# Performance work log

Measured on AMD Instinct MI355X. Metric: run time of the kernel, lower is better.

The kernel has to match this reference:

```python
import jax, jax.numpy as jnp
import numpy as np

NEG_SLOPE = 0.2
CONV3_NUM, CONV1_NUM, POLY_NUM = 3, 5, 4
FEAT_DIM = CONV3_NUM * 84 + CONV1_NUM * 12 + POLY_NUM * 12  # 360
DN = ('NCHW', 'OIHW', 'NCHW')


def leaky_relu(x):
    return jnp.where(x >= 0, x, NEG_SLOPE * x)


def conv3x3(x, feat):
    # per-sample dynamic 3x3 conv: feat[:, :81] -> kernel [3,3,3,3], feat[:, 81:84] -> bias
    B = x.shape[0]
    k = feat[:, :81].reshape(B, 3, 3, 3, 3)
    b = feat[:, 81:84]

    def one(xi, ki, bi):
        y = jax.lax.conv_general_dilated(xi[None], ki, (1, 1), 'SAME', dimension_numbers=DN)[0]
        return y + bi[:, None, None]

    return leaky_relu(jax.vmap(one)(x, k, b))


def conv1x1(x, feat):
    B = x.shape[0]
    k = feat[:, :9].reshape(B, 3, 3, 1, 1)
    b = feat[:, 9:12]

    def one(xi, ki, bi):
        y = jax.lax.conv_general_dilated(xi[None], ki, (1, 1), 'VALID', dimension_numbers=DN)[0]
        return y + bi[:, None, None]

    return leaky_relu(jax.vmap(one)(x, k, b))


def conv_stack(x, feature):
    residual = x
    for i in range(CONV3_NUM):
        x = conv3x3(x, feature[:, i * 84:(i + 1) * 84])
    off = CONV3_NUM * 84
    for i in range(CONV1_NUM):
        x = conv1x1(x, feature[:, off + i * 12:off + (i + 1) * 12])
    return residual + x


def att_map(feat, h_mat, w_mat, xc):
    # product over POLY_NUM of (a*h + b*w + c*x + d)
    att = jnp.ones_like(xc)
    for i in range(POLY_NUM):
        a = feat[:, i * 4 + 0].reshape(-1, 1, 1, 1)
        b = feat[:, i * 4 + 1].reshape(-1, 1, 1, 1)
        c = feat[:, i * 4 + 2].reshape(-1, 1, 1, 1)
        d = feat[:, i * 4 + 3].reshape(-1, 1, 1, 1)
        att = att * (a * h_mat + b * w_mat + c * xc + d)
    return att


def apply_attention(x, feature):
    H, W = x.shape[2], x.shape[3]
    h_mat = (jnp.arange(H, dtype=x.dtype) / H).reshape(1, 1, H, 1)
    w_mat = (jnp.arange(W, dtype=x.dtype) / W).reshape(1, 1, 1, W)
    off = CONV3_NUM * 84 + CONV1_NUM * 12
    atts = [att_map(feature[:, off + c * POLY_NUM * 4: off + (c + 1) * POLY_NUM * 4],
                    h_mat, w_mat, x[:, c:c + 1]) for c in range(3)]  # R, G, B
    att = jnp.concatenate(atts, axis=1)
    return x * (1 + att)


def setup_inputs() -> dict:
    key = jax.random.key(0)
    k1, k2, k3 = jax.random.split(key, 3)
    x = jax.random.uniform(k1, (8, 3, 512, 512), dtype=jnp.float32)
    thumb_x = jax.random.uniform(k2, (8, 3, 64, 64), dtype=jnp.float32)
    Wm = jax.random.normal(k3, (3, FEAT_DIM), dtype=jnp.float32) * 0.05
    bm = jnp.zeros((FEAT_DIM,), dtype=jnp.float32)
    return {"x": x, "thumb_x": thumb_x, "Wm": Wm, "bm": bm}


def reference(x, thumb_x, Wm, bm):
    # meta: GAP over thumbnail -> linear -> per-sample hypernetwork features [B, 360]
    feature = jnp.mean(thumb_x, axis=(2, 3)) @ Wm + bm
    x = conv_stack(x, feature)
    x = apply_attention(x, feature)
    thumb = conv_stack(thumb_x, feature)
    thumb = apply_attention(thumb, feature)
    return (x, thumb)
```

## Files before the change

kernel.cpp:

```cpp
#include <hip/hip_runtime.h>


#define LEAKY(v) fmaxf((v), 0.2f * (v))

constexpr int STRD = 84;
constexpr int ROWS0 = 22;
constexpr int CHS  = ROWS0 * STRD;
constexpr int BUFSZ = 3 * CHS + 16;

__global__ __launch_bounds__(384) void prep_kernel(
    const float* __restrict__ thumb, const float* __restrict__ Wm,
    const float* __restrict__ bm, float* __restrict__ feat)
{
    const int b = blockIdx.x;
    const int t = threadIdx.x;
    const int ch = t >> 7;
    const int l  = t & 127;
    const float4* p = (const float4*)(thumb + (size_t)b * 3 * 4096);
    float s = 0.f;
#pragma unroll
    for (int k = 0; k < 8; ++k) {
        float4 v = p[ch * 1024 + l + k * 128];
        s += v.x + v.y + v.z + v.w;
    }
    __shared__ float red[384];
    red[t] = s;
    __syncthreads();
    for (int off = 64; off > 0; off >>= 1) {
        if (l < off) red[t] += red[t + off];
        __syncthreads();
    }
    if (t < 360) {
        const float sc = 1.f / 4096.f;
        const float m0 = red[0] * sc, m1 = red[128] * sc, m2 = red[256] * sc;
        feat[b * 360 + t] =
            fmaf(m0, Wm[t], fmaf(m1, Wm[360 + t], fmaf(m2, Wm[720 + t], bm[t])));
    }
}

template<int R>
__device__ __forceinline__ void conv_rows(
    const float* __restrict__ buf, const float* __restrict__ fw,
    int r0, int gx, float4 acc[][3])
{
    const float b0 = fw[81], b1 = fw[82], b2 = fw[83];
#pragma unroll
    for (int j = 0; j < R; ++j) {
        acc[j][0] = make_float4(b0, b0, b0, b0);
        acc[j][1] = make_float4(b1, b1, b1, b1);
        acc[j][2] = make_float4(b2, b2, b2, b2);
    }
    const int gA = (gx < 0) ? 0 : gx;
#pragma unroll
    for (int ich = 0; ich < 3; ++ich) {
#pragma unroll
        for (int ri = 0; ri < R + 2; ++ri) {
            const int idx = ich * CHS + (r0 + 2 + ri) * STRD;
            const float4 A = *(const float4*)&buf[idx + gA];
            const float4 B = *(const float4*)&buf[idx + gx + 4];
            const float4 C = *(const float4*)&buf[idx + gx + 8];
#pragma unroll
            for (int j = 0; j < R; ++j) {
                const int dy = ri - j;
                if (dy < 0 || dy > 2) continue;
#pragma unroll
                for (int oc = 0; oc < 3; ++oc) {
                    const float w0 = fw[oc * 27 + ich * 9 + dy * 3 + 0];
                    const float w1 = fw[oc * 27 + ich * 9 + dy * 3 + 1];
                    const float w2 = fw[oc * 27 + ich * 9 + dy * 3 + 2];
                    float4& a = acc[j][oc];
                    a.x = fmaf(A.w, w0, fmaf(B.x, w1, fmaf(B.y, w2, a.x)));
                    a.y = fmaf(B.x, w0, fmaf(B.y, w1, fmaf(B.z, w2, a.y)));
                    a.z = fmaf(B.y, w0, fmaf(B.z, w1, fmaf(B.w, w2, a.z)));
                    a.w = fmaf(B.z, w0, fmaf(B.w, w1, fmaf(C.x, w2, a.w)));
                }
            }
        }
    }
}

__global__ __launch_bounds__(256, 4) void conv_att_kernel(
    const float* __restrict__ x, const float* __restrict__ thumb,
    const float* __restrict__ feat, float* __restrict__ out)
{
    __shared__ float buf[BUFSZ];

    int id = blockIdx.x;
    const float* src; float* dst; int H, W, b, trow, tcol;
    if (id < 2048) {
        b = id >> 8; const int t = id & 255;
        H = 512; W = 512; trow = (t >> 3) * 16; tcol = (t & 7) * 64;
        src = x; dst = out;
    } else {
        const int i2 = id - 2048;
        b = i2 >> 2; trow = (i2 & 3) * 16; tcol = 0;
        H = 64; W = 64; src = thumb;
        dst = out + (size_t)8 * 3 * 512 * 512;
    }
    const float* fb = feat + b * 360;
    const int tid = threadIdx.x;

    const float* sbg = src + (size_t)b * 3 * H * W;
    for (int q = tid; q < 1188; q += 256) {
        const int c = q / 396;
        const int rem = q - c * 396;
        const int mr = rem / 18;
        const int mq = rem - mr * 18;
        const int gr = trow + mr - 3;
        const int gc0 = tcol + 4 * mq - 4;
        const bool rok = (unsigned)gr < (unsigned)H;
        const float* gp = sbg + (size_t)c * H * W + (size_t)(rok ? gr : 0) * W;
        float4 v;
        if (rok && (unsigned)gc0 <= (unsigned)(W - 4)) {
            v = *(const float4*)&gp[gc0];
        } else {
            v.x = (rok && (unsigned)(gc0 + 0) < (unsigned)W) ? gp[gc0 + 0] : 0.f;
            v.y = (rok && (unsigned)(gc0 + 1) < (unsigned)W) ? gp[gc0 + 1] : 0.f;
            v.z = (rok && (unsigned)(gc0 + 2) < (unsigned)W) ? gp[gc0 + 2] : 0.f;
            v.w = (rok && (unsigned)(gc0 + 3) < (unsigned)W) ? gp[gc0 + 3] : 0.f;
        }
        *(float4*)&buf[c * CHS + mr * STRD + 4 * mq] = v;
    }
    if (tid < 66) {
        const int c = tid / 22, mr = tid - c * 22;
        *(float4*)&buf[c * CHS + mr * STRD + 72] = make_float4(0.f, 0.f, 0.f, 0.f);
    }
    __syncthreads();

    const int s3 = tid >> 4;
    const int gx3 = 4 * (tid & 15);

    const bool act1 = tid < 180;
    const int s1 = tid / 18;
    const int gx1 = 4 * (tid - s1 * 18) - 4;
    float4 acc[2][3];
    if (act1) conv_rows<2>(buf, fb, 2 * s1 - 2, gx1, acc);

    float4 res[3];
#pragma unroll
    for (int c = 0; c < 3; ++c)
        res[c] = *(const float4*)&buf[c * CHS + (s3 + 3) * STRD + gx3 + 4];
    __syncthreads();

    if (act1) {
        const int r0 = 2 * s1 - 2;
#pragma unroll
        for (int j = 0; j < 2; ++j)
#pragma unroll
            for (int oc = 0; oc < 3; ++oc) {
                float4 v = acc[j][oc];
                v.x = LEAKY(v.x); v.y = LEAKY(v.y); v.z = LEAKY(v.z); v.w = LEAKY(v.w);
                *(float4*)&buf[oc * CHS + (r0 + j + 3) * STRD + gx1 + 4] = v;
            }
    }
    __syncthreads();

    const bool act2 = tid < 162;
    const int s2 = tid / 18;
    const int gx2 = 4 * (tid - s2 * 18) - 4;
    if (act2) conv_rows<2>(buf, fb + 84, 2 * s2 - 1, gx2, acc);
    __syncthreads();

    if (act2) {
        const int r0 = 2 * s2 - 1;
#pragma unroll
        for (int j = 0; j < 2; ++j)
#pragma unroll
            for (int oc = 0; oc < 3; ++oc) {
                float4 v = acc[j][oc];
                v.x = LEAKY(v.x); v.y = LEAKY(v.y); v.z = LEAKY(v.z); v.w = LEAKY(v.w);
                *(float4*)&buf[oc * CHS + (r0 + j + 3) * STRD + gx2 + 4] = v;
            }
    }
    __syncthreads();

    float4 y[1][3];
    conv_rows<1>(buf, fb + 168, s3, gx3, y);
    float4 y0 = y[0][0], y1 = y[0][1], y2 = y[0][2];
    y0.x = LEAKY(y0.x); y0.y = LEAKY(y0.y); y0.z = LEAKY(y0.z); y0.w = LEAKY(y0.w);
    y1.x = LEAKY(y1.x); y1.y = LEAKY(y1.y); y1.z = LEAKY(y1.z); y1.w = LEAKY(y1.w);
    y2.x = LEAKY(y2.x); y2.y = LEAKY(y2.y); y2.z = LEAKY(y2.z); y2.w = LEAKY(y2.w);

#pragma unroll
    for (int lay = 0; lay < 5; ++lay) {
        const float* fw = fb + 252 + lay * 12;
        const float w00 = fw[0], w01 = fw[1], w02 = fw[2];
        const float w10 = fw[3], w11 = fw[4], w12 = fw[5];
        const float w20 = fw[6], w21 = fw[7], w22 = fw[8];
        const float c0 = fw[9], c1 = fw[10], c2 = fw[11];
        float4 z0, z1, z2;
        z0.x = fmaf(y0.x, w00, fmaf(y1.x, w01, fmaf(y2.x, w02, c0)));
        z0.y = fmaf(y0.y, w00, fmaf(y1.y, w01, fmaf(y2.y, w02, c0)));
        z0.z = fmaf(y0.z, w00, fmaf(y1.z, w01, fmaf(y2.z, w02, c0)));
        z0.w = fmaf(y0.w, w00, fmaf(y1.w, w01, fmaf(y2.w, w02, c0)));
        z1.x = fmaf(y0.x, w10, fmaf(y1.x, w11, fmaf(y2.x, w12, c1)));
        z1.y = fmaf(y0.y, w10, fmaf(y1.y, w11, fmaf(y2.y, w12, c1)));
        z1.z = fmaf(y0.z, w10, fmaf(y1.z, w11, fmaf(y2.z, w12, c1)));
        z1.w = fmaf(y0.w, w10, fmaf(y1.w, w11, fmaf(y2.w, w12, c1)));
        z2.x = fmaf(y0.x, w20, fmaf(y1.x, w21, fmaf(y2.x, w22, c2)));
        z2.y = fmaf(y0.y, w20, fmaf(y1.y, w21, fmaf(y2.y, w22, c2)));
        z2.z = fmaf(y0.z, w20, fmaf(y1.z, w21, fmaf(y2.z, w22, c2)));
        z2.w = fmaf(y0.w, w20, fmaf(y1.w, w21, fmaf(y2.w, w22, c2)));
        y0.x = LEAKY(z0.x); y0.y = LEAKY(z0.y); y0.z = LEAKY(z0.z); y0.w = LEAKY(z0.w);
        y1.x = LEAKY(z1.x); y1.y = LEAKY(z1.y); y1.z = LEAKY(z1.z); y1.w = LEAKY(z1.w);
        y2.x = LEAKY(z2.x); y2.y = LEAKY(z2.y); y2.z = LEAKY(z2.z); y2.w = LEAKY(z2.w);
    }

    const float invH = 1.f / (float)H;
    const float invW = 1.f / (float)W;
    const int gr = trow + s3;
    const float h = (float)gr * invH;
    const float wbase = (float)(tcol + gx3) * invW;
    const float4 wv = make_float4(wbase, wbase + invW, wbase + 2.f * invW, wbase + 3.f * invW);
#pragma unroll
    for (int ch = 0; ch < 3; ++ch) {
        const float* fp = fb + 312 + ch * 16;
        const float pa0 = fp[0], pb0 = fp[1], pc0 = fp[2], pd0 = fp[3];
        const float pa1 = fp[4], pb1 = fp[5], pc1 = fp[6], pd1 = fp[7];
        const float pa2 = fp[8], pb2 = fp[9], pc2 = fp[10], pd2 = fp[11];
        const float pa3 = fp[12], pb3 = fp[13], pc3 = fp[14], pd3 = fp[15];
        const float4 yv = (ch == 0) ? y0 : (ch == 1) ? y1 : y2;
        float4 v;
        v.x = yv.x + res[ch].x;
        v.y = yv.y + res[ch].y;
        v.z = yv.z + res[ch].z;
        v.w = yv.w + res[ch].w;
        const float t0 = fmaf(pa0, h, pd0), t1 = fmaf(pa1, h, pd1);
        const float t2 = fmaf(pa2, h, pd2), t3 = fmaf(pa3, h, pd3);
        float4 o;
        float a0 = fmaf(pb0, wv.x, fmaf(pc0, v.x, t0));
        a0 *= fmaf(pb1, wv.x, fmaf(pc1, v.x, t1));
        a0 *= fmaf(pb2, wv.x, fmaf(pc2, v.x, t2));
        a0 *= fmaf(pb3, wv.x, fmaf(pc3, v.x, t3));
        o.x = v.x * (1.f + a0);
        float a1 = fmaf(pb0, wv.y, fmaf(pc0, v.y, t0));
        a1 *= fmaf(pb1, wv.y, fmaf(pc1, v.y, t1));
        a1 *= fmaf(pb2, wv.y, fmaf(pc2, v.y, t2));
        a1 *= fmaf(pb3, wv.y, fmaf(pc3, v.y, t3));
        o.y = v.y * (1.f + a1);
        float a2 = fmaf(pb0, wv.z, fmaf(pc0, v.z, t0));
        a2 *= fmaf(pb1, wv.z, fmaf(pc1, v.z, t1));
        a2 *= fmaf(pb2, wv.z, fmaf(pc2, v.z, t2));
        a2 *= fmaf(pb3, wv.z, fmaf(pc3, v.z, t3));
        o.z = v.z * (1.f + a2);
        float a3 = fmaf(pb0, wv.w, fmaf(pc0, v.w, t0));
        a3 *= fmaf(pb1, wv.w, fmaf(pc1, v.w, t1));
        a3 *= fmaf(pb2, wv.w, fmaf(pc2, v.w, t2));
        a3 *= fmaf(pb3, wv.w, fmaf(pc3, v.w, t3));
        o.w = v.w * (1.f + a3);
        *(float4*)&dst[((size_t)(b * 3 + ch) * H + gr) * W + tcol + gx3] = o;
    }
}

extern "C" void kernel_launch(void* const* d_in, const int* in_sizes, int n_in,
                              void* d_out, int out_size, void* d_ws, size_t ws_size,
                              hipStream_t stream) {
    const float* x = (const float*)d_in[0];
    const float* thumb = (const float*)d_in[1];
    const float* Wm = (const float*)d_in[2];
    const float* bm = (const float*)d_in[3];
    float* out = (float*)d_out;
    float* feat = (float*)d_ws;

    prep_kernel<<<8, 384, 0, stream>>>(thumb, Wm, bm, feat);
    conv_att_kernel<<<2080, 256, 0, stream>>>(x, thumb, feat, out);
}
```

Baseline: 114.4 us.

## Widen conv tiles to 120 columns to cut halo recompute overhead

Widens each block's tile from 64 to 120 output columns (5 column tiles per 16-row band), with a 132-float shared-memory row stride. The smaller grid gives each thread extra work passes for the first two conv layers and two passes for the final stage. The wider tile lowers the fraction of halo loads and halo recomputation across the three chained 3x3 convs. The residual is now re-read from global memory instead of being kept from shared memory, and the larger shared buffer plus partial passes may cut occupancy or add idle lanes.

```diff
diff --git a/kernel.cpp b/kernel.cpp
--- a/kernel.cpp
+++ b/kernel.cpp
@@ -3,10 +3,10 @@
 
 #define LEAKY(v) fmaxf((v), 0.2f * (v))
 
-constexpr int STRD = 84;
+constexpr int STRD = 132;
 constexpr int ROWS0 = 22;
 constexpr int CHS  = ROWS0 * STRD;
-constexpr int BUFSZ = 3 * CHS + 16;
+constexpr int BUFSZ = 3 * CHS + 4;
 
 __global__ __launch_bounds__(384) void prep_kernel(
     const float* __restrict__ thumb, const float* __restrict__ Wm,
@@ -50,15 +50,15 @@
         acc[j][1] = make_float4(b1, b1, b1, b1);
         acc[j][2] = make_float4(b2, b2, b2, b2);
     }
-    const int gA = (gx < 0) ? 0 : gx;
+    const int gA = (gx == 0) ? 0 : gx - 4;
 #pragma unroll
     for (int ich = 0; ich < 3; ++ich) {
 #pragma unroll
         for (int ri = 0; ri < R + 2; ++ri) {
             const int idx = ich * CHS + (r0 + 2 + ri) * STRD;
             const float4 A = *(const float4*)&buf[idx + gA];
-            const float4 B = *(const float4*)&buf[idx + gx + 4];
-            const float4 C = *(const float4*)&buf[idx + gx + 8];
+            const float4 B = *(const float4*)&buf[idx + gx];
+            const float4 C = *(const float4*)&buf[idx + gx + 4];
 #pragma unroll
             for (int j = 0; j < R; ++j) {
                 const int dy = ri - j;
@@ -79,6 +79,19 @@
     }
 }
 
+__device__ __forceinline__ void write_strip(
+    float* __restrict__ buf, int r0, int gx, float4 acc[][3])
+{
+#pragma unroll
+    for (int j = 0; j < 2; ++j)
+#pragma unroll
+        for (int oc = 0; oc < 3; ++oc) {
+            float4 v = acc[j][oc];
+            v.x = LEAKY(v.x); v.y = LEAKY(v.y); v.z = LEAKY(v.z); v.w = LEAKY(v.w);
+            *(float4*)&buf[oc * CHS + (r0 + j + 3) * STRD + gx] = v;
+        }
+}
+
 __global__ __launch_bounds__(256, 4) void conv_att_kernel(
     const float* __restrict__ x, const float* __restrict__ thumb,
     const float* __restrict__ feat, float* __restrict__ out)
@@ -87,12 +100,13 @@
 
     int id = blockIdx.x;
     const float* src; float* dst; int H, W, b, trow, tcol;
-    if (id < 2048) {
-        b = id >> 8; const int t = id & 255;
-        H = 512; W = 512; trow = (t >> 3) * 16; tcol = (t & 7) * 64;
+    if (id < 1280) {
+        b = id / 160; const int t = id - b * 160;
+        const int band = t / 5, ct = t - band * 5;
+        H = 512; W = 512; trow = band * 16; tcol = ct * 120;
         src = x; dst = out;
     } else {
-        const int i2 = id - 2048;
+        const int i2 = id - 1280;
         b = i2 >> 2; trow = (i2 & 3) * 16; tcol = 0;
         H = 64; W = 64; src = thumb;
         dst = out + (size_t)8 * 3 * 512 * 512;
@@ -101,11 +115,11 @@
     const int tid = threadIdx.x;
 
     const float* sbg = src + (size_t)b * 3 * H * W;
-    for (int q = tid; q < 1188; q += 256) {
-        const int c = q / 396;
-        const int rem = q - c * 396;
-        const int mr = rem / 18;
-        const int mq = rem - mr * 18;
+    for (int q = tid; q < 2178; q += 256) {
+        const int c = q / 726;
+        const int rem = q - c * 726;
+        const int mr = rem / 33;
+        const int mq = rem - mr * 33;
         const int gr = trow + mr - 3;
         const int gc0 = tcol + 4 * mq - 4;
         const bool rok = (unsigned)gr < (unsigned)H;
@@ -121,134 +135,140 @@
         }
         *(float4*)&buf[c * CHS + mr * STRD + 4 * mq] = v;
     }
-    if (tid < 66) {
-        const int c = tid / 22, mr = tid - c * 22;
-        *(float4*)&buf[c * CHS + mr * STRD + 72] = make_float4(0.f, 0.f, 0.f, 0.f);
-    }
-    __syncthreads();
-
-    const int s3 = tid >> 4;
-    const int gx3 = 4 * (tid & 15);
-
-    const bool act1 = tid < 180;
-    const int s1 = tid / 18;
-    const int gx1 = 4 * (tid - s1 * 18) - 4;
-    float4 acc[2][3];
-    if (act1) conv_rows<2>(buf, fb, 2 * s1 - 2, gx1, acc);
-
-    float4 res[3];
-#pragma unroll
-    for (int c = 0; c < 3; ++c)
-        res[c] = *(const float4*)&buf[c * CHS + (s3 + 3) * STRD + gx3 + 4];
-    __syncthreads();
-
-    if (act1) {
-        const int r0 = 2 * s1 - 2;
-#pragma unroll
-        for (int j = 0; j < 2; ++j)
-#pragma unroll
-            for (int oc = 0; oc < 3; ++oc) {
-                float4 v = acc[j][oc];
-                v.x = LEAKY(v.x); v.y = LEAKY(v.y); v.z = LEAKY(v.z); v.w = LEAKY(v.w);
-                *(float4*)&buf[oc * CHS + (r0 + j + 3) * STRD + gx1 + 4] = v;
-            }
-    }
-    __syncthreads();
-
-    const bool act2 = tid < 162;
-    const int s2 = tid / 18;
-    const int gx2 = 4 * (tid - s2 * 18) - 4;
-    if (act2) conv_rows<2>(buf, fb + 84, 2 * s2 - 1, gx2, acc);
-    __syncthreads();
-
-    if (act2) {
-        const int r0 = 2 * s2 - 1;
-#pragma unroll
-        for (int j = 0; j < 2; ++j)
-#pragma unroll
-            for (int oc = 0; oc < 3; ++oc) {
-                float4 v = acc[j][oc];
-                v.x = LEAKY(v.x); v.y = LEAKY(v.y); v.z = LEAKY(v.z); v.w = LEAKY(v.w);
-                *(float4*)&buf[oc * CHS + (r0 + j + 3) * STRD + gx2 + 4] = v;
-            }
-    }
-    __syncthreads();
-
-    float4 y[1][3];
-    conv_rows<1>(buf, fb + 168, s3, gx3, y);
-    float4 y0 = y[0][0], y1 = y[0][1], y2 = y[0][2];
-    y0.x = LEAKY(y0.x); y0.y = LEAKY(y0.y); y0.z = LEAKY(y0.z); y0.w = LEAKY(y0.w);
-    y1.x = LEAKY(y1.x); y1.y = LEAKY(y1.y); y1.z = LEAKY(y1.z); y1.w = LEAKY(y1.w);
-    y2.x = LEAKY(y2.x); y2.y = LEAKY(y2.y); y2.z = LEAKY(y2.z); y2.w = LEAKY(y2.w);
-
-#pragma unroll
-    for (int lay = 0; lay < 5; ++lay) {
-        const float* fw = fb + 252 + lay * 12;
-        const float w00 = fw[0], w01 = fw[1], w02 = fw[2];
-        const float w10 = fw[3], w11 = fw[4], w12 = fw[5];
-        const float w20 = fw[6], w21 = fw[7], w22 = fw[8];
-        const float c0 = fw[9], c1 = fw[10], c2 = fw[11];
-        float4 z0, z1, z2;
-        z0.x = fmaf(y0.x, w00, fmaf(y1.x, w01, fmaf(y2.x, w02, c0)));
-        z0.y = fmaf(y0.y, w00, fmaf(y1.y, w01, fmaf(y2.y, w02, c0)));
-        z0.z = fmaf(y0.z, w00, fmaf(y1.z, w01, fmaf(y2.z, w02, c0)));
-        z0.w = fmaf(y0.w, w00, fmaf(y1.w, w01, fmaf(y2.w, w02, c0)));
-        z1.x = fmaf(y0.x, w10, fmaf(y1.x, w11, fmaf(y2.x, w12, c1)));
-        z1.y = fmaf(y0.y, w10, fmaf(y1.y, w11, fmaf(y2.y, w12, c1)));
-        z1.z = fmaf(y0.z, w10, fmaf(y1.z, w11, fmaf(y2.z, w12, c1)));
-        z1.w = fmaf(y0.w, w10, fmaf(y1.w, w11, fmaf(y2.w, w12, c1)));
-        z2.x = fmaf(y0.x, w20, fmaf(y1.x, w21, fmaf(y2.x, w22, c2)));
-        z2.y = fmaf(y0.y, w20, fmaf(y1.y, w21, fmaf(y2.y, w22, c2)));
-        z2.z = fmaf(y0.z, w20, fmaf(y1.z, w21, fmaf(y2.z, w22, c2)));
-        z2.w = fmaf(y0.w, w20, fmaf(y1.w, w21, fmaf(y2.w, w22, c2)));
-        y0.x = LEAKY(z0.x); y0.y = LEAKY(z0.y); y0.z = LEAKY(z0.z); y0.w = LEAKY(z0.w);
-        y1.x = LEAKY(z1.x); y1.y = LEAKY(z1.y); y1.z = LEAKY(z1.z); y1.w = LEAKY(z1.w);
-        y2.x = LEAKY(z2.x); y2.y = LEAKY(z2.y); y2.z = LEAKY(z2.z); y2.w = LEAKY(z2.w);
-    }
+    __syncthreads();
+
+    float4 acc1[2][3], acc2[2][3];
+    {
+        const int s = tid >> 5, g = tid & 31;
+        conv_rows<2>(buf, fb, 2 * s - 2, 4 * g, acc1);
+    }
+    const bool p2a = tid < 64;
+    if (p2a) {
+        const int u = tid + 256;
+        const int s = u >> 5, g = u & 31;
+        conv_rows<2>(buf, fb, 2 * s - 2, 4 * g, acc2);
+    }
+    __syncthreads();
+    {
+        const int s = tid >> 5, g = tid & 31;
+        write_strip(buf, 2 * s - 2, 4 * g, acc1);
+        if (p2a) {
+            const int u = tid + 256;
+            const int s2 = u >> 5, g2 = u & 31;
+            write_strip(buf, 2 * s2 - 2, 4 * g2, acc2);
+        }
+    }
+    __syncthreads();
+
+    {
+        const int s = tid >> 5, g = tid & 31;
+        conv_rows<2>(buf, fb + 84, 2 * s - 1, 4 * g, acc1);
+    }
+    const bool p2b = tid < 32;
+    if (p2b) {
+        const int u = tid + 256;
+        const int s = u >> 5, g = u & 31;
+        conv_rows<2>(buf, fb + 84, 2 * s - 1, 4 * g, acc2);
+    }
+    __syncthreads();
+    {
+        const int s = tid >> 5, g = tid & 31;
+        write_strip(buf, 2 * s - 1, 4 * g, acc1);
+        if (p2b) {
+            const int u = tid + 256;
+            const int s2 = u >> 5, g2 = u & 31;
+            write_strip(buf, 2 * s2 - 1, 4 * g2, acc2);
+        }
+    }
+    __syncthreads();
 
     const float invH = 1.f / (float)H;
     const float invW = 1.f / (float)W;
-    const int gr = trow + s3;
-    const float h = (float)gr * invH;
-    const float wbase = (float)(tcol + gx3) * invW;
-    const float4 wv = make_float4(wbase, wbase + invW, wbase + 2.f * invW, wbase + 3.f * invW);
-#pragma unroll
-    for (int ch = 0; ch < 3; ++ch) {
-        const float* fp = fb + 312 + ch * 16;
-        const float pa0 = fp[0], pb0 = fp[1], pc0 = fp[2], pd0 = fp[3];
-        const float pa1 = fp[4], pb1 = fp[5], pc1 = fp[6], pd1 = fp[7];
-        const float pa2 = fp[8], pb2 = fp[9], pc2 = fp[10], pd2 = fp[11];
-        const float pa3 = fp[12], pb3 = fp[13], pc3 = fp[14], pd3 = fp[15];
-        const float4 yv = (ch == 0) ? y0 : (ch == 1) ? y1 : y2;
-        float4 v;
-        v.x = yv.x + res[ch].x;
-        v.y = yv.y + res[ch].y;
-        v.z = yv.z + res[ch].z;
-        v.w = yv.w + res[ch].w;
-        const float t0 = fmaf(pa0, h, pd0), t1 = fmaf(pa1, h, pd1);
-        const float t2 = fmaf(pa2, h, pd2), t3 = fmaf(pa3, h, pd3);
-        float4 o;
-        float a0 = fmaf(pb0, wv.x, fmaf(pc0, v.x, t0));
-        a0 *= fmaf(pb1, wv.x, fmaf(pc1, v.x, t1));
-        a0 *= fmaf(pb2, wv.x, fmaf(pc2, v.x, t2));
-        a0 *= fmaf(pb3, wv.x, fmaf(pc3, v.x, t3));
-        o.x = v.x * (1.f + a0);
-        float a1 = fmaf(pb0, wv.y, fmaf(pc0, v.y, t0));
-        a1 *= fmaf(pb1, wv.y, fmaf(pc1, v.y, t1));
-        a1 *= fmaf(pb2, wv.y, fmaf(pc2, v.y, t2));
-        a1 *= fmaf(pb3, wv.y, fmaf(pc3, v.y, t3));
-        o.y = v.y * (1.f + a1);
-        float a2 = fmaf(pb0, wv.z, fmaf(pc0, v.z, t0));
-        a2 *= fmaf(pb1, wv.z, fmaf(pc1, v.z, t1));
-        a2 *= fmaf(pb2, wv.z, fmaf(pc2, v.z, t2));
-        a2 *= fmaf(pb3, wv.z, fmaf(pc3, v.z, t3));
-        o.z = v.z * (1.f + a2);
-        float a3 = fmaf(pb0, wv.w, fmaf(pc0, v.w, t0));
-        a3 *= fmaf(pb1, wv.w, fmaf(pc1, v.w, t1));
-        a3 *= fmaf(pb2, wv.w, fmaf(pc2, v.w, t2));
-        a3 *= fmaf(pb3, wv.w, fmaf(pc3, v.w, t3));
-        o.w = v.w * (1.f + a3);
-        *(float4*)&dst[((size_t)(b * 3 + ch) * H + gr) * W + tcol + gx3] = o;
+#pragma unroll
+    for (int pass = 0; pass < 2; ++pass) {
+        const int u = tid + pass * 256;
+        const int s3 = u >> 5;
+        const int gq = u & 31;
+        float4 y[1][3];
+        conv_rows<1>(buf, fb + 168, s3, 4 * gq, y);
+        float4 y0 = y[0][0], y1 = y[0][1], y2 = y[0][2];
+        y0.x = LEAKY(y0.x); y0.y = LEAKY(y0.y); y0.z = LEAKY(y0.z); y0.w = LEAKY(y0.w);
+        y1.x = LEAKY(y1.x); y1.y = LEAKY(y1.y); y1.z = LEAKY(y1.z); y1.w = LEAKY(y1.w);
+        y2.x = LEAKY(y2.x); y2.y = LEAKY(y2.y); y2.z = LEAKY(y2.z); y2.w = LEAKY(y2.w);
+
+#pragma unroll
+        for (int lay = 0; lay < 5; ++lay) {
+            const float* fw = fb + 252 + lay * 12;
+            const float w00 = fw[0], w01 = fw[1], w02 = fw[2];
+            const float w10 = fw[3], w11 = fw[4], w12 = fw[5];
+            const float w20 = fw[6], w21 = fw[7], w22 = fw[8];
+            const float c0 = fw[9], c1 = fw[10], c2 = fw[11];
+            float4 z0, z1, z2;
+            z0.x = fmaf(y0.x, w00, fmaf(y1.x, w01, fmaf(y2.x, w02, c0)));
+            z0.y = fmaf(y0.y, w00, fmaf(y1.y, w01, fmaf(y2.y, w02, c0)));
+            z0.z = fmaf(y0.z, w00, fmaf(y1.z, w01, fmaf(y2.z, w02, c0)));
+            z0.w = fmaf(y0.w, w00, fmaf(y1.w, w01, fmaf(y2.w, w02, c0)));
+            z1.x = fmaf(y0.x, w10, fmaf(y1.x, w11, fmaf(y2.x, w12, c1)));
+            z1.y = fmaf(y0.y, w10, fmaf(y1.y, w11, fmaf(y2.y, w12, c1)));
+            z1.z = fmaf(y0.z, w10, fmaf(y1.z, w11, fmaf(y2.z, w12, c1)));
+            z1.w = fmaf(y0.w, w10, fmaf(y1.w, w11, fmaf(y2.w, w12, c1)));
+            z2.x = fmaf(y0.x, w20, fmaf(y1.x, w21, fmaf(y2.x, w22, c2)));
+            z2.y = fmaf(y0.y, w20, fmaf(y1.y, w21, fmaf(y2.y, w22, c2)));
+            z2.z = fmaf(y0.z, w20, fmaf(y1.z, w21, fmaf(y2.z, w22, c2)));
+            z2.w = fmaf(y0.w, w20, fmaf(y1.w, w21, fmaf(y2.w, w22, c2)));
+            y0.x = LEAKY(z0.x); y0.y = LEAKY(z0.y); y0.z = LEAKY(z0.z); y0.w = LEAKY(z0.w);
+            y1.x = LEAKY(z1.x); y1.y = LEAKY(z1.y); y1.z = LEAKY(z1.z); y1.w = LEAKY(z1.w);
+            y2.x = LEAKY(z2.x); y2.y = LEAKY(z2.y); y2.z = LEAKY(z2.z); y2.w = LEAKY(z2.w);
+        }
+
+        const int gr = trow + s3;
+        const int c0i = tcol + 4 * gq - 4;
+        if (gq >= 1 && c0i <= W - 4) {
+            const float h = (float)gr * invH;
+            const float wbase = (float)c0i * invW;
+            const float4 wv = make_float4(wbase, wbase + invW,
+                                          wbase + 2.f * invW, wbase + 3.f * invW);
+#pragma unroll
+            for (int ch = 0; ch < 3; ++ch) {
+                const float4 res =
+                    *(const float4*)&sbg[(size_t)ch * H * W + (size_t)gr * W + c0i];
+                const float* fp = fb + 312 + ch * 16;
+                const float pa0 = fp[0], pb0 = fp[1], pc0 = fp[2], pd0 = fp[3];
+                const float pa1 = fp[4], pb1 = fp[5], pc1 = fp[6], pd1 = fp[7];
+                const float pa2 = fp[8], pb2 = fp[9], pc2 = fp[10], pd2 = fp[11];
+                const float pa3 = fp[12], pb3 = fp[13], pc3 = fp[14], pd3 = fp[15];
+                const float4 yv = (ch == 0) ? y0 : (ch == 1) ? y1 : y2;
+                float4 v;
+                v.x = yv.x + res.x;
+                v.y = yv.y + res.y;
+                v.z = yv.z + res.z;
+                v.w = yv.w + res.w;
+                const float t0 = fmaf(pa0, h, pd0), t1 = fmaf(pa1, h, pd1);
+                const float t2 = fmaf(pa2, h, pd2), t3 = fmaf(pa3, h, pd3);
+                float4 o;
+                float a0 = fmaf(pb0, wv.x, fmaf(pc0, v.x, t0));
+                a0 *= fmaf(pb1, wv.x, fmaf(pc1, v.x, t1));
+                a0 *= fmaf(pb2, wv.x, fmaf(pc2, v.x, t2));
+                a0 *= fmaf(pb3, wv.x, fmaf(pc3, v.x, t3));
+                o.x = v.x * (1.f + a0);
+                float a1 = fmaf(pb0, wv.y, fmaf(pc0, v.y, t0));
+                a1 *= fmaf(pb1, wv.y, fmaf(pc1, v.y, t1));
+                a1 *= fmaf(pb2, wv.y, fmaf(pc2, v.y, t2));
+                a1 *= fmaf(pb3, wv.y, fmaf(pc3, v.y, t3));
+                o.y = v.y * (1.f + a1);
+                float a2 = fmaf(pb0, wv.z, fmaf(pc0, v.z, t0));
+                a2 *= fmaf(pb1, wv.z, fmaf(pc1, v.z, t1));
+                a2 *= fmaf(pb2, wv.z, fmaf(pc2, v.z, t2));
+                a2 *= fmaf(pb3, wv.z, fmaf(pc3, v.z, t3));
+                o.z = v.z * (1.f + a2);
+                float a3 = fmaf(pb0, wv.w, fmaf(pc0, v.w, t0));
+                a3 *= fmaf(pb1, wv.w, fmaf(pc1, v.w, t1));
+                a3 *= fmaf(pb2, wv.w, fmaf(pc2, v.w, t2));
+                a3 *= fmaf(pb3, wv.w, fmaf(pc3, v.w, t3));
+                o.w = v.w * (1.f + a3);
+                *(float4*)&dst[((size_t)(b * 3 + ch) * H + gr) * W + c0i] = o;
+            }
+        }
     }
 }
 
@@ -263,5 +283,5 @@
     float* feat = (float*)d_ws;
 
     prep_kernel<<<8, 384, 0, stream>>>(thumb, Wm, bm, feat);
-    conv_att_kernel<<<2080, 256, 0, stream>>>(x, thumb, feat, out);
-}
+    conv_att_kernel<<<1312, 256, 0, stream>>>(x, thumb, feat, out);
+}
```

After: 155.8 us. 36.1% more time.
